# Kernel optimization log

Measured on AMD Instinct MI355X. Metric: run time of the kernel, lower is better.

## Reference

```python
import jax, jax.numpy as jnp
import numpy as np

D_MODEL = 1024
H = 16
D_K = D_MODEL // H
B, S = 2, 2048


def setup_inputs() -> dict:
    key = jax.random.key(0)
    ks = jax.random.split(key, 13)
    sc = 1.0 / np.sqrt(D_MODEL)
    inp = {
        "x": jax.random.normal(ks[0], (B, S, D_MODEL), jnp.float32),
        "q": jax.random.normal(ks[1], (B, S, D_MODEL), jnp.float32),
        "k": jax.random.normal(ks[2], (B, S, D_MODEL), jnp.float32),
        "v": jax.random.normal(ks[3], (B, S, D_MODEL), jnp.float32),
        "mask": jnp.ones((1, 1, S, S), jnp.int32),
        "w_q": jax.random.normal(ks[4], (D_MODEL, D_MODEL), jnp.float32) * sc,
        "b_q": jax.random.normal(ks[5], (D_MODEL,), jnp.float32) * sc,
        "w_k": jax.random.normal(ks[6], (D_MODEL, D_MODEL), jnp.float32) * sc,
        "b_k": jax.random.normal(ks[7], (D_MODEL,), jnp.float32) * sc,
        "w_v": jax.random.normal(ks[8], (D_MODEL, D_MODEL), jnp.float32) * sc,
        "b_v": jax.random.normal(ks[9], (D_MODEL,), jnp.float32) * sc,
        "w_o": jax.random.normal(ks[10], (D_MODEL, D_MODEL), jnp.float32) * sc,
        "b_o": jax.random.normal(ks[11], (D_MODEL,), jnp.float32) * sc,
    }
    return inp


def reference(x, q, k, v, mask, w_q, b_q, w_k, b_k, w_v, b_v, w_o, b_o):
    # Faithful to source bugs: value projected with w_k (not w_v);
    # mask and dropout have no effect (non-in-place / broken calls); x unused.
    query = q @ w_q.T + b_q                     # [B,S,D]
    key_p = k @ w_k.T + b_k                     # [B,S,D]
    value = v @ w_k.T + b_k                     # BUG in source: uses w_k
    # split heads -> [B,H,S,d_k]
    qh = query.reshape(B, S, H, D_K).transpose(0, 2, 1, 3)
    kh = key_p.reshape(B, S, H, D_K).transpose(0, 2, 1, 3)
    vh = value.reshape(B, S, H, D_K).transpose(0, 2, 1, 3)
    scores = jnp.einsum("bhqd,bhkd->bhqk", qh, kh) / jnp.sqrt(jnp.float32(D_K))
    attn = jax.nn.softmax(scores, axis=-1)      # [B,H,S,S]
    out = jnp.einsum("bhqk,bhkd->bhqd", attn, vh)
    out = out.transpose(0, 2, 1, 3).reshape(B, S, D_MODEL)
    return out @ w_o.T + b_o
```

## Files before the change

kernel.cpp:

```cpp
#include <hip/hip_runtime.h>

typedef unsigned short u16;
typedef __attribute__((ext_vector_type(8))) __bf16 bf16x8;
typedef __attribute__((ext_vector_type(4))) float f32x4;
typedef __attribute__((ext_vector_type(16))) float f32x16;
typedef __attribute__((ext_vector_type(8))) u16 u16x8;
typedef __attribute__((ext_vector_type(4))) u16 u16x4;
typedef __attribute__((ext_vector_type(4))) unsigned u32x4;

#define AS1 __attribute__((address_space(1)))
#define AS3 __attribute__((address_space(3)))

#if __has_builtin(__builtin_amdgcn_exp2f)
#define EXP2(x) __builtin_amdgcn_exp2f(x)
#else
#define EXP2(x) exp2f(x)
#endif

__device__ __forceinline__ u16 f2bf(float f) {
  union { float f; unsigned u; } cv; cv.f = f;
  return (u16)((cv.u + 0x7FFFu + ((cv.u >> 16) & 1u)) >> 16);
}

__device__ __forceinline__ void gload16(const void* g, void* l) {
  __builtin_amdgcn_global_load_lds((AS1 const void*)g, (AS3 void*)l, 16, 0, 0);
}

__device__ __forceinline__ unsigned cvtpk(float lo, float hi_) {
  unsigned d;
  asm("v_cvt_pk_bf16_f32 %0, %1, %2" : "=v"(d) : "v"(lo), "v"(hi_));
  return d;
}

__device__ __forceinline__ int lds_off(int row, int chunk) {
  return row * 64 + ((chunk ^ (row & 7)) << 3);
}

__global__ void cvt_kernel(const float* __restrict__ s0, u16* __restrict__ d0, int n0,
                           const float* __restrict__ s1, u16* __restrict__ d1, int n1,
                           const float* __restrict__ s2, u16* __restrict__ d2, int n2,
                           const float* __restrict__ s3, u16* __restrict__ d3, int n3,
                           const float* __restrict__ s4, u16* __restrict__ d4, int n4,
                           const float* __restrict__ s5, u16* __restrict__ d5, int n5) {
  const float* s; u16* d; int n;
  switch (blockIdx.y) {
    case 0: s = s0; d = d0; n = n0; break;
    case 1: s = s1; d = d1; n = n1; break;
    case 2: s = s2; d = d2; n = n2; break;
    case 3: s = s3; d = d3; n = n3; break;
    case 4: s = s4; d = d4; n = n4; break;
    default: s = s5; d = d5; n = n5; break;
  }
  const int stride = gridDim.x * blockDim.x;
  for (int i = blockIdx.x * blockDim.x + threadIdx.x; i < n; i += stride) {
    const float4* p = (const float4*)(s + (size_t)i * 8);
    float4 a = p[0], b = p[1];
    u16x8 r;
    r[0] = f2bf(a.x); r[1] = f2bf(a.y); r[2] = f2bf(a.z); r[3] = f2bf(a.w);
    r[4] = f2bf(b.x); r[5] = f2bf(b.y); r[6] = f2bf(b.z); r[7] = f2bf(b.w);
    *(u16x8*)(d + (size_t)i * 8) = r;
  }
}

__device__ __forceinline__ void gemm_core(const u16* __restrict__ A,
                                          const u16* __restrict__ Bm,
                                          u16* As, u16* Bs,
                                          int rowBase, int colBase,
                                          f32x4 acc[4][4]) {
  const int tid = threadIdx.x;
  const int lane = tid & 63, w = tid >> 6;
  const int wr = w >> 1, wc = w & 1;
  const int l15 = lane & 15, g = lane >> 4;

  auto stage = [&](int step, int buf) {
    const int kt = step * 32;
#pragma unroll
    for (int it = 0; it < 2; ++it) {
      int e = it * 256 + tid;
      int r = e >> 2, kc = (e & 3) << 3;
      gload16(A + (((size_t)(rowBase + r)) << 10) + kt + kc, As + buf * 4096 + e * 8);
      gload16(Bm + (((size_t)(colBase + r)) << 10) + kt + kc, Bs + buf * 4096 + e * 8);
    }
  };

  stage(0, 0);
  stage(1, 1);

  int cb = 0, nb = 2;
  for (int i = 0; i < 32; ++i) {
    if (i < 31) {
      asm volatile("s_waitcnt vmcnt(4)" ::: "memory");
    } else {
      asm volatile("s_waitcnt vmcnt(0)" ::: "memory");
    }
    __builtin_amdgcn_sched_barrier(0);
    __builtin_amdgcn_s_barrier();
    __builtin_amdgcn_sched_barrier(0);
    if (i < 30) stage(i + 2, nb);

    const u16* Ab = As + cb * 4096;
    const u16* Bb = Bs + cb * 4096;
    bf16x8 a[4], b[4];
#pragma unroll
    for (int mt = 0; mt < 4; ++mt)
      a[mt] = *(const bf16x8*)(Ab + (wr * 64 + mt * 16 + l15) * 32 + g * 8);
#pragma unroll
    for (int nt = 0; nt < 4; ++nt)
      b[nt] = *(const bf16x8*)(Bb + (wc * 64 + nt * 16 + l15) * 32 + g * 8);
#pragma unroll
    for (int mt = 0; mt < 4; ++mt)
#pragma unroll
      for (int nt = 0; nt < 4; ++nt)
        acc[mt][nt] = __builtin_amdgcn_mfma_f32_16x16x32_bf16(a[mt], b[nt], acc[mt][nt], 0, 0, 0);

    cb = cb == 2 ? 0 : cb + 1;
    nb = nb == 2 ? 0 : nb + 1;
  }
}

__global__ __launch_bounds__(256)
void proj_gemm(const u16* __restrict__ qb, const u16* __restrict__ kb, const u16* __restrict__ vb,
               const u16* __restrict__ wqb, const u16* __restrict__ wkb,
               const float* __restrict__ b_q, const float* __restrict__ b_k,
               u16* __restrict__ Qp, u16* __restrict__ Kp, u16* __restrict__ VTp) {
  __shared__ __align__(16) u16 As[3][128 * 32];
  __shared__ __align__(16) u16 Bs[3][128 * 32];

  const u16* A; const u16* Bm; const float* bias; u16* C; int mode;
  float scale = 1.0f;
  if (blockIdx.z == 0)      { A = qb; Bm = wqb; bias = b_q; C = Qp;  mode = 0; scale = 0.18033688011112042f; }
  else if (blockIdx.z == 1) { A = kb; Bm = wkb; bias = b_k; C = Kp;  mode = 0; }
  else                      { A = vb; Bm = wkb; bias = b_k; C = VTp; mode = 1; }

  const int rowBase = blockIdx.x * 128;
  const int colBase = blockIdx.y * 128;
  f32x4 acc[4][4];
  const f32x4 z4 = {0.f, 0.f, 0.f, 0.f};
#pragma unroll
  for (int i = 0; i < 4; ++i)
#pragma unroll
    for (int j = 0; j < 4; ++j) acc[i][j] = z4;

  gemm_core(A, Bm, &As[0][0], &Bs[0][0], rowBase, colBase, acc);

  const int tid = threadIdx.x;
  const int lane = tid & 63, w = tid >> 6;
  const int wr = w >> 1, wc = w & 1;
  const int l15 = lane & 15, g = lane >> 4;
#pragma unroll
  for (int mt = 0; mt < 4; ++mt)
#pragma unroll
    for (int nt = 0; nt < 4; ++nt) {
      int col = colBase + wc * 64 + nt * 16 + l15;
      float bia = bias[col];
#pragma unroll
      for (int r = 0; r < 4; ++r) {
        int row = rowBase + wr * 64 + mt * 16 + g * 4 + r;
        float val = (acc[mt][nt][r] + bia) * scale;
        if (mode == 0) {
          C[(((size_t)row) << 10) + col] = f2bf(val);
        } else {
          int bb = row >> 11, s = row & 2047;
          int s2 = s ^ ((((s >> 2) ^ (s >> 3)) & 1) * 12);
          int hh = col >> 6, d = col & 63;
          C[((((size_t)(bb * 16 + hh)) << 6) + d) * 2048 + s2] = f2bf(val);
        }
      }
    }
}

__global__ __launch_bounds__(256)
void out_gemm(const u16* __restrict__ AO, const u16* __restrict__ wob,
              const float* __restrict__ b_o, float* __restrict__ C) {
  __shared__ __align__(16) u16 As[3][64 * 32];
  __shared__ __align__(16) u16 Bs[3][128 * 32];
  const int rowBase = blockIdx.x * 64;
  const int colBase = blockIdx.y * 128;

  const int tid = threadIdx.x;
  const int lane = tid & 63, w = tid >> 6;
  const int wr = w >> 1, wc = w & 1;
  const int l15 = lane & 15, g = lane >> 4;

  auto stage = [&](int step, int buf) {
    const int kt = step * 32;
    {
      int r = tid >> 2, kc = (tid & 3) << 3;
      gload16(AO + (((size_t)(rowBase + r)) << 10) + kt + kc, &As[buf][tid * 8]);
    }
#pragma unroll
    for (int it = 0; it < 2; ++it) {
      int e = it * 256 + tid;
      int r = e >> 2, kc = (e & 3) << 3;
      gload16(wob + (((size_t)(colBase + r)) << 10) + kt + kc, &Bs[buf][e * 8]);
    }
  };

  f32x4 acc[2][4];
  const f32x4 z4 = {0.f, 0.f, 0.f, 0.f};
#pragma unroll
  for (int i = 0; i < 2; ++i)
#pragma unroll
    for (int j = 0; j < 4; ++j) acc[i][j] = z4;

  stage(0, 0);
  stage(1, 1);

  int cb = 0, nb = 2;
  for (int i = 0; i < 32; ++i) {
    if (i < 31) {
      asm volatile("s_waitcnt vmcnt(6)" ::: "memory");
    } else {
      asm volatile("s_waitcnt vmcnt(0)" ::: "memory");
    }
    __builtin_amdgcn_sched_barrier(0);
    __builtin_amdgcn_s_barrier();
    __builtin_amdgcn_sched_barrier(0);
    if (i < 30) stage(i + 2, nb);

    bf16x8 a[2], b[4];
#pragma unroll
    for (int mt = 0; mt < 2; ++mt)
      a[mt] = *(const bf16x8*)(&As[cb][(wr * 32 + mt * 16 + l15) * 32 + g * 8]);
#pragma unroll
    for (int nt = 0; nt < 4; ++nt)
      b[nt] = *(const bf16x8*)(&Bs[cb][(wc * 64 + nt * 16 + l15) * 32 + g * 8]);
#pragma unroll
    for (int mt = 0; mt < 2; ++mt)
#pragma unroll
      for (int nt = 0; nt < 4; ++nt)
        acc[mt][nt] = __builtin_amdgcn_mfma_f32_16x16x32_bf16(a[mt], b[nt], acc[mt][nt], 0, 0, 0);

    cb = cb == 2 ? 0 : cb + 1;
    nb = nb == 2 ? 0 : nb + 1;
  }

#pragma unroll
  for (int mt = 0; mt < 2; ++mt)
#pragma unroll
    for (int nt = 0; nt < 4; ++nt) {
      int col = colBase + wc * 64 + nt * 16 + l15;
      float bia = b_o[col];
#pragma unroll
      for (int r = 0; r < 4; ++r) {
        int row = rowBase + wr * 32 + mt * 16 + g * 4 + r;
        C[(((size_t)row) << 10) + col] = acc[mt][nt][r] + bia;
      }
    }
}

template <int KS4>
__device__ __forceinline__ void pv_step(const f32x16& sv, int hi, const u16* Vt, int l31,
                                        f32x16& o0, f32x16& o1) {
  constexpr int B = (KS4 & 1) * 8;
  u32x4 pd;
  pd[0] = cvtpk(sv[B + 0], sv[B + 1]);
  pd[1] = cvtpk(sv[B + 2], sv[B + 3]);
  pd[2] = cvtpk(sv[B + 4], sv[B + 5]);
  pd[3] = cvtpk(sv[B + 6], sv[B + 7]);
  bf16x8 pfrag = __builtin_bit_cast(bf16x8, pd);
  bf16x8 av0 = *(const bf16x8*)(Vt + lds_off(l31, 2 * KS4 + hi));
  bf16x8 av1 = *(const bf16x8*)(Vt + lds_off(32 + l31, 2 * KS4 + hi));
  o0 = __builtin_amdgcn_mfma_f32_32x32x16_bf16(av0, pfrag, o0, 0, 0, 0);
  o1 = __builtin_amdgcn_mfma_f32_32x32x16_bf16(av1, pfrag, o1, 0, 0, 0);
}

__global__ __launch_bounds__(512, 4)
void flash_attn(const u16* __restrict__ Qp, const u16* __restrict__ Kp,
                const u16* __restrict__ VT, u16* __restrict__ AO) {
  __shared__ __align__(16) u16 KB[2][2][64 * 64];
  __shared__ __align__(16) u16 VB[2][2][64 * 64];
  __shared__ float shML[2][256];

  const int tid = threadIdx.x;
  const int lane = tid & 63;
  const int w = tid >> 6;
  const int h = w >> 2;
  const int wq = w & 3;
  const int l31 = lane & 31;
  const int hi = lane >> 5;
  const int tid256 = tid & 255;

  const int flat = blockIdx.x + (blockIdx.y << 4);
  const int wgid = (flat & 7) * 64 + (flat >> 3);
  const int bh = wgid >> 4;
  const int qblk = wgid & 15;
  const int b = bh >> 4, hd = bh & 15;
  const int q = qblk * 128 + wq * 32 + l31;

  const size_t qrow = ((size_t)(b * 2048 + q)) << 10;
  const u16* Kbase = Kp + (((size_t)(b * 2048)) << 10) + hd * 64;
  const u16* Vbase = VT + (((size_t)(bh * 64)) << 11);

  const int sr = tid256 >> 3;
  const int sc = (tid256 & 7) ^ (sr & 7);

  auto stage = [&](int tt, int buf) {
    const int kv0 = tt * 64;
    gload16(Kbase + (((size_t)(kv0 + sr)) << 10) + sc * 8, &KB[h][buf][tid256 * 8]);
    gload16(Kbase + (((size_t)(kv0 + 32 + sr)) << 10) + sc * 8, &KB[h][buf][2048 + tid256 * 8]);
    gload16(Vbase + sr * 2048 + kv0 + sc * 8, &VB[h][buf][tid256 * 8]);
    gload16(Vbase + (32 + sr) * 2048 + kv0 + sc * 8, &VB[h][buf][2048 + tid256 * 8]);
  };

  stage(h * 16, 0);

  bf16x8 qf[4];
#pragma unroll
  for (int ks = 0; ks < 4; ++ks)
    qf[ks] = *(const bf16x8*)(Qp + qrow + hd * 64 + ks * 16 + hi * 8);

  float m = -1e30f, l = 0.f;
  f32x16 o0, o1;
#pragma unroll
  for (int i = 0; i < 16; ++i) { o0[i] = 0.f; o1[i] = 0.f; }

  for (int lt = 0; lt < 16; ++lt) {
    const int cb = lt & 1;
    asm volatile("s_waitcnt vmcnt(0)" ::: "memory");
    __builtin_amdgcn_sched_barrier(0);
    __builtin_amdgcn_s_barrier();
    __builtin_amdgcn_sched_barrier(0);
    if (lt < 15) stage(h * 16 + lt + 1, cb ^ 1);

    const u16* Kt = &KB[h][cb][0];
    const u16* Vt = &VB[h][cb][0];

    f32x16 s0, s1;
#pragma unroll
    for (int i = 0; i < 16; ++i) { s0[i] = 0.f; s1[i] = 0.f; }
#pragma unroll
    for (int ks = 0; ks < 4; ++ks) {
      bf16x8 ak0 = *(const bf16x8*)(Kt + lds_off(l31, 2 * ks + hi));
      bf16x8 ak1 = *(const bf16x8*)(Kt + lds_off(32 + l31, 2 * ks + hi));
      s0 = __builtin_amdgcn_mfma_f32_32x32x16_bf16(ak0, qf[ks], s0, 0, 0, 0);
      s1 = __builtin_amdgcn_mfma_f32_32x32x16_bf16(ak1, qf[ks], s1, 0, 0, 0);
    }

    f32x16 mm;
#pragma unroll
    for (int i = 0; i < 16; ++i) mm[i] = fmaxf(s0[i], s1[i]);
#pragma unroll
    for (int i = 0; i < 8; ++i) mm[i] = fmaxf(mm[i], mm[i + 8]);
#pragma unroll
    for (int i = 0; i < 4; ++i) mm[i] = fmaxf(mm[i], mm[i + 4]);
    float pm = fmaxf(fmaxf(mm[0], mm[1]), fmaxf(mm[2], mm[3]));
    pm = fmaxf(pm, __shfl_xor(pm, 32));

    if (!__all(pm - m <= 11.0f)) {
      float mn = fmaxf(m, pm);
      float fr = EXP2(m - mn);
      m = mn;
      l *= fr;
#pragma unroll
      for (int i = 0; i < 16; ++i) { o0[i] *= fr; o1[i] *= fr; }
    }

#pragma unroll
    for (int i = 0; i < 16; ++i) {
      s0[i] = EXP2(s0[i] - m);
      s1[i] = EXP2(s1[i] - m);
    }
#pragma unroll
    for (int i = 0; i < 16; ++i) mm[i] = s0[i] + s1[i];
#pragma unroll
    for (int i = 0; i < 8; ++i) mm[i] += mm[i + 8];
#pragma unroll
    for (int i = 0; i < 4; ++i) mm[i] += mm[i + 4];
    float ps = (mm[0] + mm[1]) + (mm[2] + mm[3]);
    ps += __shfl_xor(ps, 32);
    l += ps;

    pv_step<0>(s0, hi, Vt, l31, o0, o1);
    pv_step<1>(s0, hi, Vt, l31, o0, o1);
    pv_step<2>(s1, hi, Vt, l31, o0, o1);
    pv_step<3>(s1, hi, Vt, l31, o0, o1);
  }

  const int wl = wq * 64 + lane;
  float* shO0 = (float*)&KB[1][0][0];
  float* shO1 = (float*)&VB[1][0][0];
  if (h == 1) {
#pragma unroll
    for (int i = 0; i < 16; ++i) {
      shO0[i * 256 + wl] = o0[i];
      shO1[i * 256 + wl] = o1[i];
    }
    shML[0][wl] = m;
    shML[1][wl] = l;
  }
  __syncthreads();
  if (h == 0) {
    float mb = shML[0][wl], lb = shML[1][wl];
    float M = fmaxf(m, mb);
    float f0 = EXP2(m - M), f1 = EXP2(mb - M);
    float linv = 1.0f / (l * f0 + lb * f1);
#pragma unroll
    for (int i = 0; i < 16; ++i) {
      o0[i] = o0[i] * f0 + shO0[i * 256 + wl] * f1;
      o1[i] = o1[i] * f0 + shO1[i * 256 + wl] * f1;
    }
#pragma unroll
    for (int dt = 0; dt < 2; ++dt) {
      const f32x16& oo = dt ? o1 : o0;
#pragma unroll
      for (int g = 0; g < 4; ++g) {
        u16x4 pk;
#pragma unroll
        for (int r = 0; r < 4; ++r) pk[r] = f2bf(oo[g * 4 + r] * linv);
        const int d = dt * 32 + g * 8 + hi * 4;
        *(u16x4*)(AO + qrow + hd * 64 + d) = pk;
      }
    }
  }
}

extern "C" void kernel_launch(void* const* d_in, const int* in_sizes, int n_in,
                              void* d_out, int out_size, void* d_ws, size_t ws_size,
                              hipStream_t stream) {
  const float* q   = (const float*)d_in[1];
  const float* k   = (const float*)d_in[2];
  const float* v   = (const float*)d_in[3];
  const float* w_q = (const float*)d_in[5];
  const float* b_q = (const float*)d_in[6];
  const float* w_k = (const float*)d_in[7];
  const float* b_k = (const float*)d_in[8];
  const float* w_o = (const float*)d_in[11];
  const float* b_o = (const float*)d_in[12];
  float* out = (float*)d_out;

  u16* qb  = (u16*)d_ws;
  u16* kb  = qb  + 4194304;
  u16* vb  = kb  + 4194304;
  u16* wqb = vb  + 4194304;
  u16* wkb = wqb + 1048576;
  u16* wob = wkb + 1048576;
  u16* Qp  = wob + 1048576;
  u16* Kp  = Qp  + 4194304;
  u16* VTp = Kp  + 4194304;
  u16* AO  = qb;

  cvt_kernel<<<dim3(512, 6, 1), 256, 0, stream>>>(
      q, qb, 524288, k, kb, 524288, v, vb, 524288,
      w_q, wqb, 131072, w_k, wkb, 131072, w_o, wob, 131072);

  proj_gemm<<<dim3(32, 8, 3), 256, 0, stream>>>(qb, kb, vb, wqb, wkb, b_q, b_k, Qp, Kp, VTp);

  flash_attn<<<dim3(16, 32, 1), 512, 0, stream>>>(Qp, Kp, VTp, AO);

  out_gemm<<<dim3(64, 8, 1), 256, 0, stream>>>(AO, wob, b_o, out);
}
```

Baseline: 125.8 us.

## Fuse fp32-to-bf16 conversion of q/k/v activations into projection GEMM loads

The separate conversion pass for the q, k and v activations is removed. The projection GEMM now loads fp32 A tiles into registers, packs them to bf16 with v_cvt_pk_bf16_f32 and writes them to LDS, while B tiles still go through direct global-to-LDS loads. This removes a full write and reread of 3x8M bf16 elements. In exchange the GEMM reads twice the bytes for A and adds register staging, conversion work and an extra LDS wait to the pipelined main loop.

```diff
diff --git a/kernel.cpp b/kernel.cpp
--- a/kernel.cpp
+++ b/kernel.cpp
@@ -38,18 +38,12 @@
 
 __global__ void cvt_kernel(const float* __restrict__ s0, u16* __restrict__ d0, int n0,
                            const float* __restrict__ s1, u16* __restrict__ d1, int n1,
-                           const float* __restrict__ s2, u16* __restrict__ d2, int n2,
-                           const float* __restrict__ s3, u16* __restrict__ d3, int n3,
-                           const float* __restrict__ s4, u16* __restrict__ d4, int n4,
-                           const float* __restrict__ s5, u16* __restrict__ d5, int n5) {
+                           const float* __restrict__ s2, u16* __restrict__ d2, int n2) {
   const float* s; u16* d; int n;
   switch (blockIdx.y) {
     case 0: s = s0; d = d0; n = n0; break;
     case 1: s = s1; d = d1; n = n1; break;
-    case 2: s = s2; d = d2; n = n2; break;
-    case 3: s = s3; d = d3; n = n3; break;
-    case 4: s = s4; d = d4; n = n4; break;
-    default: s = s5; d = d5; n = n5; break;
+    default: s = s2; d = d2; n = n2; break;
   }
   const int stride = gridDim.x * blockDim.x;
   for (int i = blockIdx.x * blockDim.x + threadIdx.x; i < n; i += stride) {
@@ -62,91 +56,107 @@
   }
 }
 
-__device__ __forceinline__ void gemm_core(const u16* __restrict__ A,
-                                          const u16* __restrict__ Bm,
-                                          u16* As, u16* Bs,
-                                          int rowBase, int colBase,
-                                          f32x4 acc[4][4]) {
-  const int tid = threadIdx.x;
-  const int lane = tid & 63, w = tid >> 6;
-  const int wr = w >> 1, wc = w & 1;
-  const int l15 = lane & 15, g = lane >> 4;
-
-  auto stage = [&](int step, int buf) {
-    const int kt = step * 32;
-#pragma unroll
-    for (int it = 0; it < 2; ++it) {
-      int e = it * 256 + tid;
-      int r = e >> 2, kc = (e & 3) << 3;
-      gload16(A + (((size_t)(rowBase + r)) << 10) + kt + kc, As + buf * 4096 + e * 8);
-      gload16(Bm + (((size_t)(colBase + r)) << 10) + kt + kc, Bs + buf * 4096 + e * 8);
-    }
-  };
-
-  stage(0, 0);
-  stage(1, 1);
-
-  int cb = 0, nb = 2;
-  for (int i = 0; i < 32; ++i) {
-    if (i < 31) {
-      asm volatile("s_waitcnt vmcnt(4)" ::: "memory");
-    } else {
-      asm volatile("s_waitcnt vmcnt(0)" ::: "memory");
-    }
-    __builtin_amdgcn_sched_barrier(0);
-    __builtin_amdgcn_s_barrier();
-    __builtin_amdgcn_sched_barrier(0);
-    if (i < 30) stage(i + 2, nb);
-
-    const u16* Ab = As + cb * 4096;
-    const u16* Bb = Bs + cb * 4096;
-    bf16x8 a[4], b[4];
-#pragma unroll
-    for (int mt = 0; mt < 4; ++mt)
-      a[mt] = *(const bf16x8*)(Ab + (wr * 64 + mt * 16 + l15) * 32 + g * 8);
-#pragma unroll
-    for (int nt = 0; nt < 4; ++nt)
-      b[nt] = *(const bf16x8*)(Bb + (wc * 64 + nt * 16 + l15) * 32 + g * 8);
-#pragma unroll
-    for (int mt = 0; mt < 4; ++mt)
-#pragma unroll
-      for (int nt = 0; nt < 4; ++nt)
-        acc[mt][nt] = __builtin_amdgcn_mfma_f32_16x16x32_bf16(a[mt], b[nt], acc[mt][nt], 0, 0, 0);
-
-    cb = cb == 2 ? 0 : cb + 1;
-    nb = nb == 2 ? 0 : nb + 1;
-  }
-}
-
 __global__ __launch_bounds__(256)
-void proj_gemm(const u16* __restrict__ qb, const u16* __restrict__ kb, const u16* __restrict__ vb,
+void proj_gemm(const float* __restrict__ qf32, const float* __restrict__ kf32,
+               const float* __restrict__ vf32,
                const u16* __restrict__ wqb, const u16* __restrict__ wkb,
                const float* __restrict__ b_q, const float* __restrict__ b_k,
                u16* __restrict__ Qp, u16* __restrict__ Kp, u16* __restrict__ VTp) {
   __shared__ __align__(16) u16 As[3][128 * 32];
   __shared__ __align__(16) u16 Bs[3][128 * 32];
 
-  const u16* A; const u16* Bm; const float* bias; u16* C; int mode;
+  const float* A; const u16* Bm; const float* bias; u16* C; int mode;
   float scale = 1.0f;
-  if (blockIdx.z == 0)      { A = qb; Bm = wqb; bias = b_q; C = Qp;  mode = 0; scale = 0.18033688011112042f; }
-  else if (blockIdx.z == 1) { A = kb; Bm = wkb; bias = b_k; C = Kp;  mode = 0; }
-  else                      { A = vb; Bm = wkb; bias = b_k; C = VTp; mode = 1; }
+  if (blockIdx.z == 0)      { A = qf32; Bm = wqb; bias = b_q; C = Qp;  mode = 0; scale = 0.18033688011112042f; }
+  else if (blockIdx.z == 1) { A = kf32; Bm = wkb; bias = b_k; C = Kp;  mode = 0; }
+  else                      { A = vf32; Bm = wkb; bias = b_k; C = VTp; mode = 1; }
 
   const int rowBase = blockIdx.x * 128;
   const int colBase = blockIdx.y * 128;
-  f32x4 acc[4][4];
-  const f32x4 z4 = {0.f, 0.f, 0.f, 0.f};
-#pragma unroll
-  for (int i = 0; i < 4; ++i)
-#pragma unroll
-    for (int j = 0; j < 4; ++j) acc[i][j] = z4;
-
-  gemm_core(A, Bm, &As[0][0], &Bs[0][0], rowBase, colBase, acc);
 
   const int tid = threadIdx.x;
   const int lane = tid & 63, w = tid >> 6;
   const int wr = w >> 1, wc = w & 1;
   const int l15 = lane & 15, g = lane >> 4;
+
+  const int e0 = tid, e1 = 256 + tid;
+  const int r0 = e0 >> 2, kc0 = (e0 & 3) << 3;
+  const int r1 = e1 >> 2, kc1 = (e1 & 3) << 3;
+
+  float4 ar0[4], ar1[4];
+
+  auto aload = [&](int step, float4* ar) {
+    const float* p0 = A + (((size_t)(rowBase + r0)) << 10) + step * 32 + kc0;
+    const float* p1 = A + (((size_t)(rowBase + r1)) << 10) + step * 32 + kc1;
+    ar[0] = ((const float4*)p0)[0];
+    ar[1] = ((const float4*)p0)[1];
+    ar[2] = ((const float4*)p1)[0];
+    ar[3] = ((const float4*)p1)[1];
+  };
+  auto bstage = [&](int step, int buf) {
+    gload16(Bm + (((size_t)(colBase + r0)) << 10) + step * 32 + kc0, &Bs[buf][e0 * 8]);
+    gload16(Bm + (((size_t)(colBase + r1)) << 10) + step * 32 + kc1, &Bs[buf][e1 * 8]);
+  };
+  auto awrite = [&](const float4* ar, int buf) {
+    u32x4 pd0, pd1;
+    pd0[0] = cvtpk(ar[0].x, ar[0].y); pd0[1] = cvtpk(ar[0].z, ar[0].w);
+    pd0[2] = cvtpk(ar[1].x, ar[1].y); pd0[3] = cvtpk(ar[1].z, ar[1].w);
+    pd1[0] = cvtpk(ar[2].x, ar[2].y); pd1[1] = cvtpk(ar[2].z, ar[2].w);
+    pd1[2] = cvtpk(ar[3].x, ar[3].y); pd1[3] = cvtpk(ar[3].z, ar[3].w);
+    *(u32x4*)(&As[buf][e0 * 8]) = pd0;
+    *(u32x4*)(&As[buf][e1 * 8]) = pd1;
+  };
+
+  f32x4 acc[4][4];
+  const f32x4 z4 = {0.f, 0.f, 0.f, 0.f};
+#pragma unroll
+  for (int i = 0; i < 4; ++i)
+#pragma unroll
+    for (int j = 0; j < 4; ++j) acc[i][j] = z4;
+
+  aload(0, ar0); bstage(0, 0);
+  aload(1, ar1); bstage(1, 1);
+
+  for (int j = 0; j < 16; ++j) {
+#pragma unroll
+    for (int ii = 0; ii < 2; ++ii) {
+      const int i = 2 * j + ii;
+      const int buf = i % 3;
+      float4* arX = ii ? ar1 : ar0;
+
+      if (i < 31) {
+        asm volatile("s_waitcnt vmcnt(6)" ::: "memory");
+      } else {
+        asm volatile("s_waitcnt vmcnt(0)" ::: "memory");
+      }
+      __builtin_amdgcn_sched_barrier(0);
+      awrite(arX, buf);
+      asm volatile("s_waitcnt lgkmcnt(0)" ::: "memory");
+      __builtin_amdgcn_sched_barrier(0);
+      __builtin_amdgcn_s_barrier();
+      __builtin_amdgcn_sched_barrier(0);
+      if (i < 30) {
+        aload(i + 2, arX);
+        bstage(i + 2, (i + 2) % 3);
+      }
+
+      const u16* Ab = &As[buf][0];
+      const u16* Bb = &Bs[buf][0];
+      bf16x8 a[4], b[4];
+#pragma unroll
+      for (int mt = 0; mt < 4; ++mt)
+        a[mt] = *(const bf16x8*)(Ab + (wr * 64 + mt * 16 + l15) * 32 + g * 8);
+#pragma unroll
+      for (int nt = 0; nt < 4; ++nt)
+        b[nt] = *(const bf16x8*)(Bb + (wc * 64 + nt * 16 + l15) * 32 + g * 8);
+#pragma unroll
+      for (int mt = 0; mt < 4; ++mt)
+#pragma unroll
+        for (int nt = 0; nt < 4; ++nt)
+          acc[mt][nt] = __builtin_amdgcn_mfma_f32_16x16x32_bf16(a[mt], b[nt], acc[mt][nt], 0, 0, 0);
+    }
+  }
+
 #pragma unroll
   for (int mt = 0; mt < 4; ++mt)
 #pragma unroll
@@ -440,11 +450,10 @@
   u16* VTp = Kp  + 4194304;
   u16* AO  = qb;
 
-  cvt_kernel<<<dim3(512, 6, 1), 256, 0, stream>>>(
-      q, qb, 524288, k, kb, 524288, v, vb, 524288,
+  cvt_kernel<<<dim3(512, 3, 1), 256, 0, stream>>>(
       w_q, wqb, 131072, w_k, wkb, 131072, w_o, wob, 131072);
 
-  proj_gemm<<<dim3(32, 8, 3), 256, 0, stream>>>(qb, kb, vb, wqb, wkb, b_q, b_k, Qp, Kp, VTp);
+  proj_gemm<<<dim3(32, 8, 3), 256, 0, stream>>>(q, k, v, wqb, wkb, b_q, b_k, Qp, Kp, VTp);
 
   flash_attn<<<dim3(16, 32, 1), 512, 0, stream>>>(Qp, Kp, VTp, AO);
 
```

Result: slower. 144.2 us (+14.6%).
